# Kernel optimization log

Hardware: AMD Instinct MI355X
Metric: run time of the kernel (lower is better)

The kernel has to match this reference:

```python
import jax, jax.numpy as jnp
import numpy as np

B, CIN, H, W = 4, 256, 64, 64
COUT = CIN // 2  # 128
EPS = 1e-5


def setup_inputs() -> dict:
    key = jax.random.key(0)
    ks = jax.random.split(key, 10)
    s_in = 1.0 / np.sqrt(CIN)
    s_out = 1.0 / np.sqrt(COUT)
    return {
        "x": jax.random.normal(ks[0], (B, CIN, H, W), dtype=jnp.float32),
        "Wq": jax.random.uniform(ks[1], (COUT, CIN), jnp.float32, -s_in, s_in),
        "bq": jax.random.uniform(ks[2], (COUT,), jnp.float32, -s_in, s_in),
        "Wk": jax.random.uniform(ks[3], (COUT, CIN), jnp.float32, -s_in, s_in),
        "bk": jax.random.uniform(ks[4], (COUT,), jnp.float32, -s_in, s_in),
        "Wv": jax.random.uniform(ks[5], (COUT, CIN), jnp.float32, -s_in, s_in),
        "bv": jax.random.uniform(ks[6], (COUT,), jnp.float32, -s_in, s_in),
        "Ww": jax.random.uniform(ks[7], (CIN, COUT), jnp.float32, -s_out, s_out),
        "bw": jax.random.uniform(ks[8], (CIN,), jnp.float32, -s_out, s_out),
        "bn_gamma": jnp.ones((CIN,), jnp.float32),
        "bn_beta": jnp.zeros((CIN,), jnp.float32),
        "bn_mean": jnp.zeros((CIN,), jnp.float32),
        "bn_var": jnp.ones((CIN,), jnp.float32),
    }


def reference(x, Wq, bq, Wk, bk, Wv, bv, Ww, bw, bn_gamma, bn_beta, bn_mean, bn_var):
    b, c, h, w = x.shape
    n = h * w
    xf = x.reshape(b, c, n)  # [B, Cin, N]
    # 1x1 convs == channel-mixing matmuls on flattened spatial dim
    q = jnp.einsum("oc,bcn->bon", Wq, xf) + bq[None, :, None]  # [B, Cout, N]
    k = jnp.einsum("oc,bcn->bon", Wk, xf) + bk[None, :, None]
    v = jnp.einsum("oc,bcn->bon", Wv, xf) + bv[None, :, None]
    # f = k^T @ q  (no scaling, as in the original)
    f = jnp.einsum("bcn,bcm->bnm", k, q)  # [B, N, N]
    f = jax.nn.softmax(f, axis=-1)
    # y = v @ f
    y = jnp.einsum("bcn,bnm->bcm", v, f)  # [B, Cout, N]
    # output 1x1 conv + eval-mode BatchNorm + residual
    z = jnp.einsum("oc,bcn->bon", Ww, y) + bw[None, :, None]  # [B, Cin, N]
    inv = bn_gamma / jnp.sqrt(bn_var + EPS)
    z = z * inv[None, :, None] + (bn_beta - bn_mean * inv)[None, :, None]
    return z.reshape(b, c, h, w) + x
```

## Files before the change

kernel.cpp:

```cpp
#include <hip/hip_runtime.h>
#include <hip/hip_bf16.h>

#define BATCH 4
#define CIN   256
#define CMID  128
#define NPOS  4096
#define EPS   1e-5f
#define NQATT 4

typedef __bf16 bf16;
typedef __attribute__((ext_vector_type(8))) __bf16 bf16x8;
typedef __attribute__((ext_vector_type(4))) __bf16 bf16x4;
typedef __attribute__((ext_vector_type(4))) float  f32x4;

#define MFMA16(a, b, c) __builtin_amdgcn_mfma_f32_16x16x32_bf16((a), (b), (c), 0, 0, 0)

#define GLDS(gsrc, ldst) \
    __builtin_amdgcn_global_load_lds( \
        (const __attribute__((address_space(1))) void*)(gsrc), \
        (__attribute__((address_space(3))) void*)(ldst), 16, 0, 0)

__device__ __forceinline__ int swz256(int row, int colb) {
    return row * 256 + ((((colb >> 4) ^ (row & 7)) << 4) | (colb & 15));
}
__device__ __forceinline__ int swz128(int row, int colb) {
    return row * 128 + ((((colb >> 4) ^ (row & 7)) << 4) | (colb & 15));
}
__device__ __forceinline__ int cswz(int row, int n4) {
    return (row * 4 + (n4 ^ ((row >> 1) & 3))) * 16;
}

__global__ __launch_bounds__(256) void kt_transpose(const float* __restrict__ x,
                                                    bf16* __restrict__ xT) {
    __shared__ float tile[64][65];
    int n0 = blockIdx.x * 64, c0 = blockIdx.y * 64, b = blockIdx.z;
    const float* xp = x + (size_t)b * CIN * NPOS;
    int t = threadIdx.x;
    int lr = t >> 4;
    int lc4 = (t & 15) * 4;
    for (int p = 0; p < 4; ++p) {
        int c = lr + p * 16;
        f32x4 v = *reinterpret_cast<const f32x4*>(xp + (size_t)(c0 + c) * NPOS + n0 + lc4);
        tile[c][lc4 + 0] = v[0]; tile[c][lc4 + 1] = v[1];
        tile[c][lc4 + 2] = v[2]; tile[c][lc4 + 3] = v[3];
    }
    __syncthreads();
    bf16* xtp = xT + (size_t)b * NPOS * CIN;
    int cc = (t & 15) * 4;
    for (int p = 0; p < 4; ++p) {
        int n = (t >> 4) + p * 16;
        bf16x4 o;
        o[0] = (bf16)tile[cc + 0][n]; o[1] = (bf16)tile[cc + 1][n];
        o[2] = (bf16)tile[cc + 2][n]; o[3] = (bf16)tile[cc + 3][n];
        *reinterpret_cast<bf16x4*>(xtp + (size_t)(n0 + n) * CIN + c0 + cc) = o;
    }
}

__global__ __launch_bounds__(256) void k_qkv(
    const float* __restrict__ Wq, const float* __restrict__ Wk, const float* __restrict__ Wv,
    const float* __restrict__ bq, const float* __restrict__ bk, const float* __restrict__ bv,
    const bf16* __restrict__ xT, bf16* __restrict__ qT, bf16* __restrict__ kT,
    bf16* __restrict__ vC) {
    __shared__ __align__(16) char a_lds[128 * 128];
    __shared__ __align__(16) char b_lds[128 * 128];
    int n0 = blockIdx.x * 128, which = blockIdx.y, b = blockIdx.z;
    const float* W    = which == 0 ? Wq : (which == 1 ? Wk : Wv);
    const float* bias = which == 0 ? bq : (which == 1 ? bk : bv);
    int t = threadIdx.x, lane = t & 63, w = t >> 6, wy = w >> 1, wx = w & 1;
    const bf16* xb = xT + (size_t)b * NPOS * CIN;

    f32x4 acc[4][4] = {};
    for (int k0 = 0; k0 < 256; k0 += 64) {
        __syncthreads();
        for (int i = 0; i < 8; ++i) {
            int idx = t + i * 256;
            int row = idx >> 4, c4 = (idx & 15) * 4;
            f32x4 v = *reinterpret_cast<const f32x4*>(W + (size_t)row * CIN + k0 + c4);
            bf16x4 o; o[0] = (bf16)v[0]; o[1] = (bf16)v[1]; o[2] = (bf16)v[2]; o[3] = (bf16)v[3];
            *reinterpret_cast<bf16x4*>(a_lds + swz128(row, c4 * 2)) = o;
        }
        for (int i = 0; i < 4; ++i) {
            int idx = t + i * 256;
            int row = idx >> 3, cb = (idx & 7) * 16;
            bf16x8 vv = *reinterpret_cast<const bf16x8*>(xb + (size_t)(n0 + row) * CIN + k0 + cb / 2);
            *reinterpret_cast<bf16x8*>(b_lds + swz128(row, cb)) = vv;
        }
        __syncthreads();
        for (int ks = 0; ks < 2; ++ks) {
            int kb = ks * 64 + (lane >> 4) * 16;
            bf16x8 af[4], bfr[4];
            for (int i = 0; i < 4; ++i)
                af[i] = *reinterpret_cast<const bf16x8*>(a_lds + swz128(wy * 64 + i * 16 + (lane & 15), kb));
            for (int j = 0; j < 4; ++j)
                bfr[j] = *reinterpret_cast<const bf16x8*>(b_lds + swz128(wx * 64 + j * 16 + (lane & 15), kb));
            for (int i = 0; i < 4; ++i)
                for (int j = 0; j < 4; ++j)
                    acc[i][j] = MFMA16(af[i], bfr[j], acc[i][j]);
        }
    }
    int rg = lane >> 4, cl = lane & 15;
    for (int i = 0; i < 4; ++i) {
        int ch0 = wy * 64 + i * 16 + rg * 4;
        f32x4 bv4 = *reinterpret_cast<const f32x4*>(bias + ch0);
        for (int j = 0; j < 4; ++j) {
            int n = n0 + wx * 64 + j * 16 + cl;
            f32x4 d = acc[i][j];
            for (int r = 0; r < 4; ++r) d[r] += bv4[r];
            if (which == 2) {
                for (int r = 0; r < 4; ++r)
                    vC[((size_t)b * CMID + ch0 + r) * NPOS + n] = (bf16)d[r];
            } else {
                bf16x4 o; o[0] = (bf16)d[0]; o[1] = (bf16)d[1]; o[2] = (bf16)d[2]; o[3] = (bf16)d[3];
                bf16* dst = (which == 0 ? qT : kT);
                *reinterpret_cast<bf16x4*>(dst + ((size_t)b * NPOS + n) * CMID + ch0) = o;
            }
        }
    }
}

__global__ __launch_bounds__(256, 4) void k_zrow(const bf16* __restrict__ qT,
                                                 const bf16* __restrict__ kT,
                                                 float* __restrict__ zpart) {
    __shared__ __align__(16) char q_lds[2][64 * 256];
    int l = blockIdx.x;
    int xcd = l & 7, slot = l >> 3;
    int mq = xcd, b = slot & 3;
    int n0 = (slot >> 2) * 128;
    int t = threadIdx.x, lane = t & 63, w = t >> 6;
    int cl = lane & 15, g = lane >> 4;
    const bf16* qb = qT + (size_t)b * NPOS * CMID;
    const bf16* kb = kT + (size_t)b * NPOS * CMID;

    auto stage_q = [&](int buf, int m0) {
        #pragma unroll
        for (int i = 0; i < 4; ++i) {
            int lc = (w * 4 + i) * 64 + lane;
            int r = lc >> 4, p = lc & 15;
            GLDS(qb + (size_t)(m0 + r) * CMID + ((p ^ (r & 7)) << 3),
                 q_lds[buf] + (w * 4 + i) * 1024);
        }
    };

    bf16x8 kreg[2][4];
    for (int jn = 0; jn < 2; ++jn)
        for (int ks = 0; ks < 4; ++ks)
            kreg[jn][ks] = *reinterpret_cast<const bf16x8*>(
                kb + (size_t)(n0 + w * 32 + jn * 16 + cl) * CMID + ks * 32 + g * 8);

    int mbeg = mq * (NPOS / 8);
    stage_q(0, mbeg);
    asm volatile("s_waitcnt vmcnt(0)" ::: "memory");
    __syncthreads();
    int cur = 0;
    float zacc[2] = {0.f, 0.f};
    for (int m0 = mbeg; m0 < mbeg + NPOS / 8; m0 += 64) {
        if (m0 + 64 < mbeg + NPOS / 8) stage_q(cur ^ 1, m0 + 64);
        f32x4 acc[4][2] = {};
        __builtin_amdgcn_s_setprio(1);
        for (int ks = 0; ks < 4; ++ks) {
            bf16x8 qf[4];
            for (int im = 0; im < 4; ++im)
                qf[im] = *reinterpret_cast<const bf16x8*>(q_lds[cur] + swz256(im * 16 + cl, ks * 64 + g * 16));
            for (int im = 0; im < 4; ++im)
                for (int jn = 0; jn < 2; ++jn)
                    acc[im][jn] = MFMA16(qf[im], kreg[jn][ks], acc[im][jn]);
        }
        __builtin_amdgcn_s_setprio(0);
        for (int im = 0; im < 4; ++im)
            for (int jn = 0; jn < 2; ++jn)
                for (int r = 0; r < 4; ++r)
                    zacc[jn] += __expf(acc[im][jn][r]);
        __syncthreads();
        cur ^= 1;
    }
    for (int jn = 0; jn < 2; ++jn) {
        zacc[jn] += __shfl_xor(zacc[jn], 16);
        zacc[jn] += __shfl_xor(zacc[jn], 32);
    }
    if (g == 0) {
        float* zp = zpart + ((size_t)mq * BATCH + b) * NPOS;
        zp[n0 + w * 32 + cl]      = zacc[0];
        zp[n0 + w * 32 + 16 + cl] = zacc[1];
    }
}

__global__ __launch_bounds__(256) void k_rcp(const float* __restrict__ zpart,
                                             float* __restrict__ invZ) {
    int i = (blockIdx.x * 256 + threadIdx.x) * 4;
    f32x4 s = {0.f, 0.f, 0.f, 0.f};
    for (int p = 0; p < 8; ++p) {
        f32x4 a = *reinterpret_cast<const f32x4*>(zpart + (size_t)p * BATCH * NPOS + i);
        for (int r = 0; r < 4; ++r) s[r] += a[r];
    }
    f32x4 o;
    for (int r = 0; r < 4; ++r) o[r] = 1.f / s[r];
    *reinterpret_cast<f32x4*>(invZ + i) = o;
}

__global__ __launch_bounds__(256) void k_vscale(bf16* __restrict__ vC,
                                                const float* __restrict__ invZ) {
    int idx = blockIdx.x * 256 + threadIdx.x;
    int b = idx >> 16;
    int n8 = idx & (NPOS / 8 - 1);
    bf16x8 v = *reinterpret_cast<const bf16x8*>(vC + (size_t)idx * 8);
    const float* iz = invZ + (size_t)b * NPOS + n8 * 8;
    f32x4 i0 = *reinterpret_cast<const f32x4*>(iz);
    f32x4 i1 = *reinterpret_cast<const f32x4*>(iz + 4);
    bf16x8 o;
    for (int r = 0; r < 4; ++r) {
        o[r]     = (bf16)((float)v[r]     * i0[r]);
        o[r + 4] = (bf16)((float)v[r + 4] * i1[r]);
    }
    *reinterpret_cast<bf16x8*>(vC + (size_t)idx * 8) = o;
}

__global__ __launch_bounds__(256, 2) void k_attn(const bf16* __restrict__ qT,
                                                 const bf16* __restrict__ kT,
                                                 const bf16* __restrict__ vS,
                                                 bf16* __restrict__ ys) {
    __shared__ __align__(16) char k_lds[2][64 * 256];
    __shared__ __align__(16) char v_lds[2][128 * 128];
    __shared__ __align__(16) char p_lds[128 * 128];
    int l = blockIdx.x;
    int xcd = l & 7, slot = l >> 3;
    int combo = xcd * 2 + (slot & 1);
    int m0 = (slot >> 1) * 128;
    int nq = combo >> 2, b = combo & 3;
    int t = threadIdx.x, lane = t & 63, w = t >> 6;
    int cl = lane & 15, g = lane >> 4;
    const bf16* qb = qT + (size_t)b * NPOS * CMID;
    const bf16* kb = kT + (size_t)b * NPOS * CMID;
    const bf16* vb = vS + (size_t)b * CMID * NPOS;

    auto stage_kv = [&](int buf, int n0) {
        #pragma unroll
        for (int i = 0; i < 4; ++i) {
            int lc = (w * 4 + i) * 64 + lane;
            int kr = lc >> 4, kp = lc & 15;
            GLDS(kb + (size_t)(n0 + kr) * CMID + ((kp ^ (kr & 7)) << 3),
                 k_lds[buf] + (w * 4 + i) * 1024);
            int vr = lc >> 3, vp = lc & 7;
            GLDS(vb + (size_t)vr * NPOS + n0 + ((vp ^ (vr & 7)) << 3),
                 v_lds[buf] + (w * 4 + i) * 1024);
        }
    };

    bf16x8 qreg[2][4];
    for (int jm = 0; jm < 2; ++jm)
        for (int ks = 0; ks < 4; ++ks)
            qreg[jm][ks] = *reinterpret_cast<const bf16x8*>(
                qb + (size_t)(m0 + w * 32 + jm * 16 + cl) * CMID + ks * 32 + g * 8);

    f32x4 acc2[2][8] = {};
    int nbeg = nq * (NPOS / NQATT);
    stage_kv(0, nbeg);
    asm volatile("s_waitcnt vmcnt(0)" ::: "memory");
    __syncthreads();
    int cur = 0;
    for (int s = 0; s < NPOS / NQATT / 64; ++s) {
        int n0 = nbeg + s * 64;
        if (s + 1 < NPOS / NQATT / 64) stage_kv(cur ^ 1, n0 + 64);
        f32x4 acc1[4][2] = {};
        __builtin_amdgcn_s_setprio(1);
        for (int ks = 0; ks < 4; ++ks) {
            bf16x8 kf[4];
            for (int in = 0; in < 4; ++in)
                kf[in] = *reinterpret_cast<const bf16x8*>(k_lds[cur] + swz256(in * 16 + cl, ks * 64 + g * 16));
            for (int in = 0; in < 4; ++in)
                for (int jm = 0; jm < 2; ++jm)
                    acc1[in][jm] = MFMA16(kf[in], qreg[jm][ks], acc1[in][jm]);
        }
        __builtin_amdgcn_s_setprio(0);
        for (int in = 0; in < 4; ++in)
            for (int jm = 0; jm < 2; ++jm) {
                bf16x4 o;
                for (int r = 0; r < 4; ++r) o[r] = (bf16)__expf(acc1[in][jm][r]);
                *reinterpret_cast<bf16x4*>(p_lds + swz128(w * 32 + jm * 16 + cl, in * 32 + g * 8)) = o;
            }
        __builtin_amdgcn_s_setprio(1);
        for (int s32 = 0; s32 < 2; ++s32) {
            bf16x8 af[2], vf[8];
            for (int jm = 0; jm < 2; ++jm)
                af[jm] = *reinterpret_cast<const bf16x8*>(p_lds + swz128(w * 32 + jm * 16 + cl, s32 * 64 + g * 16));
            for (int j = 0; j < 8; ++j)
                vf[j] = *reinterpret_cast<const bf16x8*>(v_lds[cur] + swz128(j * 16 + cl, s32 * 64 + g * 16));
            for (int jm = 0; jm < 2; ++jm)
                for (int j = 0; j < 8; ++j)
                    acc2[jm][j] = MFMA16(af[jm], vf[j], acc2[jm][j]);
        }
        __builtin_amdgcn_s_setprio(0);
        __syncthreads();
        cur ^= 1;
    }
    bf16* yb = ys + (size_t)nq * BATCH * NPOS * CMID
             + ((size_t)b * NPOS + m0) * CMID;
    for (int jm = 0; jm < 2; ++jm)
        for (int j = 0; j < 8; ++j) {
            int c = j * 16 + cl;
            for (int r = 0; r < 4; ++r) {
                int m = w * 32 + jm * 16 + g * 4 + r;
                yb[(size_t)m * CMID + c] = (bf16)acc2[jm][j][r];
            }
        }
}

__global__ __launch_bounds__(256) void k_out(
    const float* __restrict__ Ww, const float* __restrict__ bw,
    const float* __restrict__ gamma, const float* __restrict__ beta,
    const float* __restrict__ mean, const float* __restrict__ var,
    const bf16* __restrict__ ys, int ns,
    const float* __restrict__ x, float* __restrict__ out) {
    __shared__ __align__(16) char a_lds[128 * 128];
    __shared__ __align__(16) char b_lds[64 * 128];
    int m0 = blockIdx.x * 64, o0 = blockIdx.y * 128, b = blockIdx.z;
    int t = threadIdx.x, lane = t & 63, w = t >> 6, wy = w >> 1, wx = w & 1;
    const size_t SL = (size_t)BATCH * NPOS * CMID;
    f32x4 acc[4][2] = {};
    for (int k0 = 0; k0 < 128; k0 += 64) {
        __syncthreads();
        for (int i = 0; i < 8; ++i) {
            int idx = t + i * 256, row = idx >> 4, c4 = (idx & 15) * 4;
            f32x4 v = *reinterpret_cast<const f32x4*>(Ww + (size_t)(o0 + row) * CMID + k0 + c4);
            bf16x4 o; o[0] = (bf16)v[0]; o[1] = (bf16)v[1]; o[2] = (bf16)v[2]; o[3] = (bf16)v[3];
            *reinterpret_cast<bf16x4*>(a_lds + swz128(row, c4 * 2)) = o;
        }
        for (int i = 0; i < 4; ++i) {
            int idx = t + i * 256, row = idx >> 4, c4 = (idx & 15) * 4;
            size_t yoff = ((size_t)b * NPOS + m0 + row) * CMID + k0 + c4;
            float sacc[4] = {0.f, 0.f, 0.f, 0.f};
            for (int p = 0; p < ns; ++p) {
                bf16x4 a = *reinterpret_cast<const bf16x4*>(ys + (size_t)p * SL + yoff);
                for (int r = 0; r < 4; ++r) sacc[r] += (float)a[r];
            }
            bf16x4 o;
            for (int r = 0; r < 4; ++r) o[r] = (bf16)sacc[r];
            *reinterpret_cast<bf16x4*>(b_lds + swz128(row, c4 * 2)) = o;
        }
        __syncthreads();
        for (int ks = 0; ks < 2; ++ks) {
            int kb = ks * 64 + (lane >> 4) * 16;
            bf16x8 af[4], bfr[2];
            for (int i = 0; i < 4; ++i)
                af[i] = *reinterpret_cast<const bf16x8*>(a_lds + swz128(wy * 64 + i * 16 + (lane & 15), kb));
            for (int j = 0; j < 2; ++j)
                bfr[j] = *reinterpret_cast<const bf16x8*>(b_lds + swz128(wx * 32 + j * 16 + (lane & 15), kb));
            for (int i = 0; i < 4; ++i)
                for (int j = 0; j < 2; ++j)
                    acc[i][j] = MFMA16(af[i], bfr[j], acc[i][j]);
        }
    }
    int rg = lane >> 4, cl = lane & 15;
    const float* xb = x + (size_t)b * CIN * NPOS;
    float* ob = out + (size_t)b * CIN * NPOS;
    for (int i = 0; i < 4; ++i) {
        int och0 = o0 + wy * 64 + i * 16 + rg * 4;
        f32x4 gg = *reinterpret_cast<const f32x4*>(gamma + och0);
        f32x4 be = *reinterpret_cast<const f32x4*>(beta + och0);
        f32x4 mu = *reinterpret_cast<const f32x4*>(mean + och0);
        f32x4 va = *reinterpret_cast<const f32x4*>(var + och0);
        f32x4 bb = *reinterpret_cast<const f32x4*>(bw + och0);
        float invv[4], addv[4];
        for (int r = 0; r < 4; ++r) {
            invv[r] = gg[r] / sqrtf(va[r] + EPS);
            addv[r] = be[r] - mu[r] * invv[r];
        }
        for (int j = 0; j < 2; ++j) {
            int m = m0 + wx * 32 + j * 16 + cl;
            for (int r = 0; r < 4; ++r) {
                float z = (acc[i][j][r] + bb[r]) * invv[r] + addv[r];
                ob[(size_t)(och0 + r) * NPOS + m] = z + xb[(size_t)(och0 + r) * NPOS + m];
            }
        }
    }
}

extern "C" void kernel_launch(void* const* d_in, const int* in_sizes, int n_in,
                              void* d_out, int out_size, void* d_ws, size_t ws_size,
                              hipStream_t stream) {
    const float* x     = (const float*)d_in[0];
    const float* Wq    = (const float*)d_in[1];
    const float* bq    = (const float*)d_in[2];
    const float* Wk    = (const float*)d_in[3];
    const float* bk    = (const float*)d_in[4];
    const float* Wv    = (const float*)d_in[5];
    const float* bv    = (const float*)d_in[6];
    const float* Ww    = (const float*)d_in[7];
    const float* bw    = (const float*)d_in[8];
    const float* gamma = (const float*)d_in[9];
    const float* beta  = (const float*)d_in[10];
    const float* mean  = (const float*)d_in[11];
    const float* var   = (const float*)d_in[12];
    float* out = (float*)d_out;

    const size_t slice = (size_t)BATCH * NPOS * CMID * 2;

    char* p = (char*)d_ws;
    bf16* ys = (bf16*)p;        p += (size_t)NQATT * slice;
    bf16* qT = (bf16*)p;        p += slice;
    bf16* kT = (bf16*)p;        p += slice;
    bf16* vC = (bf16*)p;        p += slice;
    float* zpart = (float*)p;   p += (size_t)8 * BATCH * NPOS * 4;
    float* invZ = (float*)p;
    bf16* xT = (bf16*)d_ws;

    kt_transpose<<<dim3(NPOS / 64, CIN / 64, BATCH), 256, 0, stream>>>(x, xT);
    k_qkv<<<dim3(NPOS / 128, 3, BATCH), 256, 0, stream>>>(Wq, Wk, Wv, bq, bk, bv, xT, qT, kT, vC);
    k_zrow<<<dim3(1024), 256, 0, stream>>>(qT, kT, zpart);
    k_rcp<<<dim3(BATCH * NPOS / 1024), 256, 0, stream>>>(zpart, invZ);
    k_vscale<<<dim3(BATCH * CMID * NPOS / 8 / 256), 256, 0, stream>>>(vC, invZ);
    k_attn<<<dim3(512), 256, 0, stream>>>(qT, kT, vC, ys);
    k_out<<<dim3(NPOS / 64, 2, BATCH), 256, 0, stream>>>(Ww, bw, gamma, beta, mean, var, ys, NQATT, x, out);
}
```

Before: 105.5 us.

## Pre-convert weights to bf16 and double-buffer QKV and output GEMMs via direct LDS loads

Adds a small kernel that converts all four weight matrices to bf16 once per call, so the QKV and output GEMMs no longer reconvert fp32 weights in every block. k_qkv now uses global_load_lds with double-buffered LDS stages so the next K-slice loads while MFMAs run. k_out is retiled so each block computes all 256 output channels for 32 positions with the whole weight matrix held in LDS. This costs an extra launch and a larger LDS footprint, which may lower occupancy in k_out.

```diff
diff --git a/kernel.cpp b/kernel.cpp
--- a/kernel.cpp
+++ b/kernel.cpp
@@ -26,8 +26,20 @@
 __device__ __forceinline__ int swz128(int row, int colb) {
     return row * 128 + ((((colb >> 4) ^ (row & 7)) << 4) | (colb & 15));
 }
-__device__ __forceinline__ int cswz(int row, int n4) {
-    return (row * 4 + (n4 ^ ((row >> 1) & 3))) * 16;
+
+__global__ __launch_bounds__(256) void k_wcvt(const float* __restrict__ Wq,
+                                              const float* __restrict__ Wk,
+                                              const float* __restrict__ Wv,
+                                              const float* __restrict__ Ww,
+                                              bf16* __restrict__ wb) {
+    int which = blockIdx.y;
+    const float* src = which == 0 ? Wq : which == 1 ? Wk : which == 2 ? Wv : Ww;
+    int i = (blockIdx.x * 256 + threadIdx.x) * 8;
+    f32x4 v0 = *reinterpret_cast<const f32x4*>(src + i);
+    f32x4 v1 = *reinterpret_cast<const f32x4*>(src + i + 4);
+    bf16x8 o;
+    for (int r = 0; r < 4; ++r) { o[r] = (bf16)v0[r]; o[r + 4] = (bf16)v1[r]; }
+    *reinterpret_cast<bf16x8*>(wb + (size_t)which * 32768 + i) = o;
 }
 
 __global__ __launch_bounds__(256) void kt_transpose(const float* __restrict__ x,
@@ -57,46 +69,52 @@
 }
 
 __global__ __launch_bounds__(256) void k_qkv(
-    const float* __restrict__ Wq, const float* __restrict__ Wk, const float* __restrict__ Wv,
+    const bf16* __restrict__ wb,
     const float* __restrict__ bq, const float* __restrict__ bk, const float* __restrict__ bv,
     const bf16* __restrict__ xT, bf16* __restrict__ qT, bf16* __restrict__ kT,
     bf16* __restrict__ vC) {
-    __shared__ __align__(16) char a_lds[128 * 128];
-    __shared__ __align__(16) char b_lds[128 * 128];
+    __shared__ __align__(16) char a_lds[2][128 * 128];
+    __shared__ __align__(16) char b_lds[2][128 * 128];
     int n0 = blockIdx.x * 128, which = blockIdx.y, b = blockIdx.z;
-    const float* W    = which == 0 ? Wq : (which == 1 ? Wk : Wv);
+    const bf16* W = wb + (size_t)which * 32768;
     const float* bias = which == 0 ? bq : (which == 1 ? bk : bv);
     int t = threadIdx.x, lane = t & 63, w = t >> 6, wy = w >> 1, wx = w & 1;
     const bf16* xb = xT + (size_t)b * NPOS * CIN;
 
+    auto stage = [&](int buf, int k0) {
+        #pragma unroll
+        for (int i = 0; i < 4; ++i) {
+            int lc = (w * 4 + i) * 64 + lane;
+            int row = lc >> 3, p = lc & 7;
+            GLDS(W + (size_t)row * CIN + k0 + ((p ^ (row & 7)) << 3),
+                 a_lds[buf] + (w * 4 + i) * 1024);
+            GLDS(xb + (size_t)(n0 + row) * CIN + k0 + ((p ^ (row & 7)) << 3),
+                 b_lds[buf] + (w * 4 + i) * 1024);
+        }
+    };
+
     f32x4 acc[4][4] = {};
-    for (int k0 = 0; k0 < 256; k0 += 64) {
-        __syncthreads();
-        for (int i = 0; i < 8; ++i) {
-            int idx = t + i * 256;
-            int row = idx >> 4, c4 = (idx & 15) * 4;
-            f32x4 v = *reinterpret_cast<const f32x4*>(W + (size_t)row * CIN + k0 + c4);
-            bf16x4 o; o[0] = (bf16)v[0]; o[1] = (bf16)v[1]; o[2] = (bf16)v[2]; o[3] = (bf16)v[3];
-            *reinterpret_cast<bf16x4*>(a_lds + swz128(row, c4 * 2)) = o;
-        }
-        for (int i = 0; i < 4; ++i) {
-            int idx = t + i * 256;
-            int row = idx >> 3, cb = (idx & 7) * 16;
-            bf16x8 vv = *reinterpret_cast<const bf16x8*>(xb + (size_t)(n0 + row) * CIN + k0 + cb / 2);
-            *reinterpret_cast<bf16x8*>(b_lds + swz128(row, cb)) = vv;
-        }
-        __syncthreads();
+    stage(0, 0);
+    asm volatile("s_waitcnt vmcnt(0)" ::: "memory");
+    __syncthreads();
+    int cur = 0;
+    for (int s = 0; s < 4; ++s) {
+        if (s < 3) stage(cur ^ 1, (s + 1) * 64);
         for (int ks = 0; ks < 2; ++ks) {
             int kb = ks * 64 + (lane >> 4) * 16;
             bf16x8 af[4], bfr[4];
             for (int i = 0; i < 4; ++i)
-                af[i] = *reinterpret_cast<const bf16x8*>(a_lds + swz128(wy * 64 + i * 16 + (lane & 15), kb));
+                af[i] = *reinterpret_cast<const bf16x8*>(a_lds[cur] + swz128(wy * 64 + i * 16 + (lane & 15), kb));
             for (int j = 0; j < 4; ++j)
-                bfr[j] = *reinterpret_cast<const bf16x8*>(b_lds + swz128(wx * 64 + j * 16 + (lane & 15), kb));
+                bfr[j] = *reinterpret_cast<const bf16x8*>(b_lds[cur] + swz128(wx * 64 + j * 16 + (lane & 15), kb));
+            __builtin_amdgcn_s_setprio(1);
             for (int i = 0; i < 4; ++i)
                 for (int j = 0; j < 4; ++j)
                     acc[i][j] = MFMA16(af[i], bfr[j], acc[i][j]);
-        }
+            __builtin_amdgcn_s_setprio(0);
+        }
+        __syncthreads();
+        cur ^= 1;
     }
     int rg = lane >> 4, cl = lane & 15;
     for (int i = 0; i < 4; ++i) {
@@ -305,55 +323,60 @@
 }
 
 __global__ __launch_bounds__(256) void k_out(
-    const float* __restrict__ Ww, const float* __restrict__ bw,
+    const bf16* __restrict__ Wwb, const float* __restrict__ bw,
     const float* __restrict__ gamma, const float* __restrict__ beta,
     const float* __restrict__ mean, const float* __restrict__ var,
     const bf16* __restrict__ ys, int ns,
     const float* __restrict__ x, float* __restrict__ out) {
-    __shared__ __align__(16) char a_lds[128 * 128];
-    __shared__ __align__(16) char b_lds[64 * 128];
-    int m0 = blockIdx.x * 64, o0 = blockIdx.y * 128, b = blockIdx.z;
-    int t = threadIdx.x, lane = t & 63, w = t >> 6, wy = w >> 1, wx = w & 1;
+    __shared__ __align__(16) char a_lds[256 * 256];
+    __shared__ __align__(16) char b_lds[32 * 256];
+    int m0 = blockIdx.x * 32, b = blockIdx.y;
+    int t = threadIdx.x, lane = t & 63, w = t >> 6;
+    int cl = lane & 15, g = lane >> 4;
     const size_t SL = (size_t)BATCH * NPOS * CMID;
+
+    #pragma unroll
+    for (int i = 0; i < 16; ++i) {
+        int lc = (w * 16 + i) * 64 + lane;
+        int row = lc >> 4, p = lc & 15;
+        GLDS(Wwb + (size_t)row * CMID + ((p ^ (row & 7)) << 3),
+             a_lds + (w * 16 + i) * 1024);
+    }
+    for (int i = 0; i < 2; ++i) {
+        int lc = t * 2 + i;
+        int row = lc >> 4, cb = (lc & 15) * 16;
+        size_t yoff = ((size_t)b * NPOS + m0 + row) * CMID + cb / 2;
+        float sacc[8] = {};
+        for (int p = 0; p < ns; ++p) {
+            bf16x8 a = *reinterpret_cast<const bf16x8*>(ys + (size_t)p * SL + yoff);
+            for (int r = 0; r < 8; ++r) sacc[r] += (float)a[r];
+        }
+        bf16x8 o;
+        for (int r = 0; r < 8; ++r) o[r] = (bf16)sacc[r];
+        *reinterpret_cast<bf16x8*>(b_lds + swz256(row, cb)) = o;
+    }
+    asm volatile("s_waitcnt vmcnt(0)" ::: "memory");
+    __syncthreads();
+
     f32x4 acc[4][2] = {};
-    for (int k0 = 0; k0 < 128; k0 += 64) {
-        __syncthreads();
-        for (int i = 0; i < 8; ++i) {
-            int idx = t + i * 256, row = idx >> 4, c4 = (idx & 15) * 4;
-            f32x4 v = *reinterpret_cast<const f32x4*>(Ww + (size_t)(o0 + row) * CMID + k0 + c4);
-            bf16x4 o; o[0] = (bf16)v[0]; o[1] = (bf16)v[1]; o[2] = (bf16)v[2]; o[3] = (bf16)v[3];
-            *reinterpret_cast<bf16x4*>(a_lds + swz128(row, c4 * 2)) = o;
-        }
-        for (int i = 0; i < 4; ++i) {
-            int idx = t + i * 256, row = idx >> 4, c4 = (idx & 15) * 4;
-            size_t yoff = ((size_t)b * NPOS + m0 + row) * CMID + k0 + c4;
-            float sacc[4] = {0.f, 0.f, 0.f, 0.f};
-            for (int p = 0; p < ns; ++p) {
-                bf16x4 a = *reinterpret_cast<const bf16x4*>(ys + (size_t)p * SL + yoff);
-                for (int r = 0; r < 4; ++r) sacc[r] += (float)a[r];
-            }
-            bf16x4 o;
-            for (int r = 0; r < 4; ++r) o[r] = (bf16)sacc[r];
-            *reinterpret_cast<bf16x4*>(b_lds + swz128(row, c4 * 2)) = o;
-        }
-        __syncthreads();
-        for (int ks = 0; ks < 2; ++ks) {
-            int kb = ks * 64 + (lane >> 4) * 16;
-            bf16x8 af[4], bfr[2];
-            for (int i = 0; i < 4; ++i)
-                af[i] = *reinterpret_cast<const bf16x8*>(a_lds + swz128(wy * 64 + i * 16 + (lane & 15), kb));
+    for (int ks = 0; ks < 4; ++ks) {
+        int kb = ks * 64 + g * 16;
+        bf16x8 af[4], bfr[2];
+        for (int i = 0; i < 4; ++i)
+            af[i] = *reinterpret_cast<const bf16x8*>(a_lds + swz256(w * 64 + i * 16 + cl, kb));
+        for (int j = 0; j < 2; ++j)
+            bfr[j] = *reinterpret_cast<const bf16x8*>(b_lds + swz256(j * 16 + cl, kb));
+        __builtin_amdgcn_s_setprio(1);
+        for (int i = 0; i < 4; ++i)
             for (int j = 0; j < 2; ++j)
-                bfr[j] = *reinterpret_cast<const bf16x8*>(b_lds + swz128(wx * 32 + j * 16 + (lane & 15), kb));
-            for (int i = 0; i < 4; ++i)
-                for (int j = 0; j < 2; ++j)
-                    acc[i][j] = MFMA16(af[i], bfr[j], acc[i][j]);
-        }
-    }
-    int rg = lane >> 4, cl = lane & 15;
+                acc[i][j] = MFMA16(af[i], bfr[j], acc[i][j]);
+        __builtin_amdgcn_s_setprio(0);
+    }
+
     const float* xb = x + (size_t)b * CIN * NPOS;
     float* ob = out + (size_t)b * CIN * NPOS;
     for (int i = 0; i < 4; ++i) {
-        int och0 = o0 + wy * 64 + i * 16 + rg * 4;
+        int och0 = w * 64 + i * 16 + g * 4;
         f32x4 gg = *reinterpret_cast<const f32x4*>(gamma + och0);
         f32x4 be = *reinterpret_cast<const f32x4*>(beta + och0);
         f32x4 mu = *reinterpret_cast<const f32x4*>(mean + och0);
@@ -365,7 +388,7 @@
             addv[r] = be[r] - mu[r] * invv[r];
         }
         for (int j = 0; j < 2; ++j) {
-            int m = m0 + wx * 32 + j * 16 + cl;
+            int m = m0 + j * 16 + cl;
             for (int r = 0; r < 4; ++r) {
                 float z = (acc[i][j][r] + bb[r]) * invv[r] + addv[r];
                 ob[(size_t)(och0 + r) * NPOS + m] = z + xb[(size_t)(och0 + r) * NPOS + m];
@@ -400,14 +423,16 @@
     bf16* kT = (bf16*)p;        p += slice;
     bf16* vC = (bf16*)p;        p += slice;
     float* zpart = (float*)p;   p += (size_t)8 * BATCH * NPOS * 4;
-    float* invZ = (float*)p;
+    float* invZ = (float*)p;    p += (size_t)BATCH * NPOS * 4;
+    bf16* wbuf = (bf16*)p;
     bf16* xT = (bf16*)d_ws;
 
+    k_wcvt<<<dim3(16, 4), 256, 0, stream>>>(Wq, Wk, Wv, Ww, wbuf);
     kt_transpose<<<dim3(NPOS / 64, CIN / 64, BATCH), 256, 0, stream>>>(x, xT);
-    k_qkv<<<dim3(NPOS / 128, 3, BATCH), 256, 0, stream>>>(Wq, Wk, Wv, bq, bk, bv, xT, qT, kT, vC);
+    k_qkv<<<dim3(NPOS / 128, 3, BATCH), 256, 0, stream>>>(wbuf, bq, bk, bv, xT, qT, kT, vC);
     k_zrow<<<dim3(1024), 256, 0, stream>>>(qT, kT, zpart);
     k_rcp<<<dim3(BATCH * NPOS / 1024), 256, 0, stream>>>(zpart, invZ);
     k_vscale<<<dim3(BATCH * CMID * NPOS / 8 / 256), 256, 0, stream>>>(vC, invZ);
     k_attn<<<dim3(512), 256, 0, stream>>>(qT, kT, vC, ys);
-    k_out<<<dim3(NPOS / 64, 2, BATCH), 256, 0, stream>>>(Ww, bw, gamma, beta, mean, var, ys, NQATT, x, out);
-}
+    k_out<<<dim3(NPOS / 32, BATCH), 256, 0, stream>>>(wbuf + 3 * 32768, bw, gamma, beta, mean, var, ys, NQATT, x, out);
+}
```

Measured after the change: 100.4 us. 4.8% less time.
